# Optimization experiments

Hardware: AMD Instinct MI355X
Metric: run time of the kernel (lower is better)

The kernel has to match this reference:

```python
import jax, jax.numpy as jnp
import numpy as np

EPS = 1e-8  # torch.nn.CosineSimilarity default eps


def _one_sided_chamfer(ex, ey):
    # ex: [N, D], ey: [M, D]
    # cosine(ex_i, ey_j) = <ex_i, ey_j> / (max(||ex_i||, eps) * max(||ey_j||, eps))
    nx = jnp.maximum(jnp.linalg.norm(ex, axis=-1, keepdims=True), EPS)  # [N,1]
    ny = jnp.maximum(jnp.linalg.norm(ey, axis=-1, keepdims=True), EPS)  # [M,1]
    exn = ex / nx
    eyn = ey / ny
    sims = jnp.einsum('nd,md->nm', exn, eyn)  # [N, M] cosine matrix
    return jnp.max(sims, axis=-1)  # row-wise max -> [N]


def setup_inputs() -> dict:
    key = jax.random.key(0)
    k1, k2 = jax.random.split(key)
    ex = jax.random.normal(k1, (8192, 768), dtype=jnp.float32)
    ey = jax.random.normal(k2, (8192, 768), dtype=jnp.float32)
    return {"ex": ex, "ey": ey}


def reference(ex, ey):
    return _one_sided_chamfer(ex, ey)
```

## Files before the change

kernel.cpp:

```cpp
#include <hip/hip_runtime.h>
#include <math.h>

#define NROWS 8192
#define KDIM  768
#define BM 128
#define BN 128
#define BKB 128
#define KTILES (KDIM / BKB)
#define NBC 4
#define NBCG (NROWS / BN / NBC)

typedef int i32x4 __attribute__((ext_vector_type(4)));

static __device__ __forceinline__ unsigned enc_f(float f) {
    unsigned x = __float_as_uint(f);
    return (x & 0x80000000u) ? ~x : (x | 0x80000000u);
}
static __device__ __forceinline__ float dec_f(unsigned u) {
    unsigned x = (u & 0x80000000u) ? (u ^ 0x80000000u) : ~u;
    return __uint_as_float(x);
}

__global__ __launch_bounds__(256) void normalize_quant_k(
        const float* __restrict__ ex, const float* __restrict__ ey,
        signed char* __restrict__ q, float* __restrict__ scales,
        unsigned* __restrict__ out) {
    if (blockIdx.x < NROWS / 256)
        out[blockIdx.x * 256 + threadIdx.x] = enc_f(-INFINITY);
    const int wave = threadIdx.x >> 6, lane = threadIdx.x & 63;
    const int grow = blockIdx.x * 4 + wave;
    const float* src = (grow < NROWS) ? ex : ey;
    const int row = grow & (NROWS - 1);
    const float4* xr = (const float4*)(src + (size_t)row * KDIM);
    float4 v[3];
    #pragma unroll
    for (int g = 0; g < 3; ++g) v[g] = xr[lane + g * 64];
    float ss = 0.f, am = 0.f;
    #pragma unroll
    for (int g = 0; g < 3; ++g) {
        ss += v[g].x * v[g].x + v[g].y * v[g].y + v[g].z * v[g].z + v[g].w * v[g].w;
        am = fmaxf(am, fmaxf(fmaxf(fabsf(v[g].x), fabsf(v[g].y)),
                             fmaxf(fabsf(v[g].z), fabsf(v[g].w))));
    }
    #pragma unroll
    for (int off = 32; off > 0; off >>= 1) {
        ss += __shfl_xor(ss, off);
        am = fmaxf(am, __shfl_xor(am, off));
    }
    const float scale = 1.0f / fmaxf(sqrtf(ss), 1e-8f);
    am = fmaxf(am * scale, 1e-12f);
    if (lane == 0) scales[grow] = am * (1.0f / 127.0f);
    const float si = scale * (127.0f / am);
    int* dr = (int*)(q + (size_t)grow * KDIM);
    #pragma unroll
    for (int g = 0; g < 3; ++g) {
        int qx = min(127, max(-127, __float2int_rn(v[g].x * si)));
        int qy = min(127, max(-127, __float2int_rn(v[g].y * si)));
        int qz = min(127, max(-127, __float2int_rn(v[g].z * si)));
        int qw = min(127, max(-127, __float2int_rn(v[g].w * si)));
        dr[lane + g * 64] = (qx & 0xff) | ((qy & 0xff) << 8) |
                            ((qz & 0xff) << 16) | ((qw & 0xff) << 24);
    }
}

__global__ __launch_bounds__(256, 4) void gemm_rowmax_i8_k(
        const signed char* __restrict__ A, const signed char* __restrict__ B,
        const float* __restrict__ sa, const float* __restrict__ sb,
        unsigned* __restrict__ out) {
    __shared__ signed char As[BM * BKB];
    __shared__ signed char Bs[BN * BKB];

    const int tid  = threadIdx.x;
    const int wave = tid >> 6, lane = tid & 63;
    const int br  = blockIdx.x >> 4;
    const int bcg = blockIdx.x & 15;

    const int srow   = lane >> 3;
    const int gchunk = (lane & 7) ^ srow;
    const int scol   = gchunk * 16;
    const signed char* aStage = A + (size_t)(br * BM + wave * 8 + srow) * KDIM + scol;
    signed char* lA = As + wave * 1024;
    signed char* lB = Bs + wave * 1024;

    const int wm = (wave >> 1) * 64, wn = (wave & 1) * 64;
    const int quad = lane >> 4, mrow = lane & 15;
    const int c0 = quad ^ (mrow & 7);
    const signed char* aBase = As + (wm + mrow) * BKB;
    const signed char* bBase = Bs + (wn + mrow) * BKB;
    const int row0 = br * BM + wm + quad * 4;

    #pragma unroll 1
    for (int bi = 0; bi < NBC; ++bi) {
        const int bc = bcg * NBC + bi;
        const signed char* bStage =
            B + (size_t)(bc * BN + wave * 8 + srow) * KDIM + scol;

        i32x4 acc[4][4] = {};

        #pragma unroll 1
        for (int kt = 0; kt < KTILES; ++kt) {
            __syncthreads();
            #pragma unroll
            for (int i = 0; i < 4; ++i) {
                __builtin_amdgcn_global_load_lds(
                    (const __attribute__((address_space(1))) void*)(aStage + kt * BKB + i * 24576),
                    (__attribute__((address_space(3))) void*)(lA + i * 4096), 16, 0, 0);
                __builtin_amdgcn_global_load_lds(
                    (const __attribute__((address_space(1))) void*)(bStage + kt * BKB + i * 24576),
                    (__attribute__((address_space(3))) void*)(lB + i * 4096), 16, 0, 0);
            }
            __syncthreads();

            #pragma unroll 1
            for (int ks = 0; ks < 2; ++ks) {
                const int ck = c0 ^ (ks << 2);
                i32x4 af[4], bfr[4];
                #pragma unroll
                for (int mi = 0; mi < 4; ++mi)
                    af[mi] = *(const i32x4*)(aBase + mi * 16 * BKB + ck * 16);
                #pragma unroll
                for (int ni = 0; ni < 4; ++ni)
                    bfr[ni] = *(const i32x4*)(bBase + ni * 16 * BKB + ck * 16);
                #pragma unroll
                for (int mi = 0; mi < 4; ++mi)
                    #pragma unroll
                    for (int ni = 0; ni < 4; ++ni)
                        acc[mi][ni] = __builtin_amdgcn_mfma_i32_16x16x64_i8(
                            af[mi], bfr[ni], acc[mi][ni], 0, 0, 0);
            }
        }

        float sbv[4];
        #pragma unroll
        for (int ni = 0; ni < 4; ++ni)
            sbv[ni] = sb[bc * BN + wn + ni * 16 + mrow];
        #pragma unroll
        for (int mi = 0; mi < 4; ++mi) {
            #pragma unroll
            for (int r = 0; r < 4; ++r) {
                float v = fmaxf(fmaxf((float)acc[mi][0][r] * sbv[0],
                                      (float)acc[mi][1][r] * sbv[1]),
                                fmaxf((float)acc[mi][2][r] * sbv[2],
                                      (float)acc[mi][3][r] * sbv[3]));
                v = fmaxf(v, __shfl_xor(v, 1));
                v = fmaxf(v, __shfl_xor(v, 2));
                v = fmaxf(v, __shfl_xor(v, 4));
                v = fmaxf(v, __shfl_xor(v, 8));
                if (mrow == 0) {
                    const int row = row0 + mi * 16 + r;
                    atomicMax(&out[row], enc_f(v * sa[row]));
                }
            }
        }
    }
}

__global__ void decode_out_k(unsigned* __restrict__ u) {
    int i = blockIdx.x * 256 + threadIdx.x;
    ((float*)u)[i] = dec_f(u[i]);
}

extern "C" void kernel_launch(void* const* d_in, const int* in_sizes, int n_in,
                              void* d_out, int out_size, void* d_ws, size_t ws_size,
                              hipStream_t stream) {
    (void)in_sizes; (void)n_in; (void)out_size; (void)ws_size;
    const float* ex = (const float*)d_in[0];
    const float* ey = (const float*)d_in[1];
    signed char* q = (signed char*)d_ws;
    float* scales  = (float*)(q + 2 * (size_t)NROWS * KDIM);
    unsigned* outu = (unsigned*)d_out;

    normalize_quant_k<<<(2 * NROWS) / 4, 256, 0, stream>>>(ex, ey, q, scales, outu);
    gemm_rowmax_i8_k<<<(NROWS / BM) * NBCG, 256, 0, stream>>>(
        q, q + (size_t)NROWS * KDIM, scales, scales + NROWS, outu);
    decode_out_k<<<NROWS / 256, 256, 0, stream>>>(outu);
}
```

Measured before the change: 165.3 us.

## Enlarge int8 GEMM tiles to 256x256 with 4-stage async LDS pipeline

Doubles the block tile to 256x256 with 512 threads (8 waves, each computing 128x64) and halves the K step to 64. Global-to-LDS loads now run three stages ahead through a four-buffer ring, gated by explicit vmcnt waits and a single barrier per step instead of two syncthreads. The goal is to hide load latency and raise arithmetic intensity. In exchange, LDS use and register pressure grow, and the grid shrinks to 256 blocks, which may underfill the GPU.

```diff
diff --git a/kernel.cpp b/kernel.cpp
--- a/kernel.cpp
+++ b/kernel.cpp
@@ -3,12 +3,12 @@
 
 #define NROWS 8192
 #define KDIM  768
-#define BM 128
-#define BN 128
-#define BKB 128
-#define KTILES (KDIM / BKB)
+#define BM 256
+#define BN 256
+#define BKB 64
+#define KT (KDIM / BKB)
 #define NBC 4
-#define NBCG (NROWS / BN / NBC)
+#define NT_ALL (NBC * KT)
 
 typedef int i32x4 __attribute__((ext_vector_type(4)));
 
@@ -63,79 +63,89 @@
     }
 }
 
-__global__ __launch_bounds__(256, 4) void gemm_rowmax_i8_k(
+__global__ __launch_bounds__(512, 2) void gemm_rowmax_i8_k(
         const signed char* __restrict__ A, const signed char* __restrict__ B,
         const float* __restrict__ sa, const float* __restrict__ sb,
         unsigned* __restrict__ out) {
-    __shared__ signed char As[BM * BKB];
-    __shared__ signed char Bs[BN * BKB];
+    __shared__ __attribute__((aligned(128))) signed char As[4][BM * BKB];
+    __shared__ __attribute__((aligned(128))) signed char Bs[4][BN * BKB];
 
     const int tid  = threadIdx.x;
     const int wave = tid >> 6, lane = tid & 63;
-    const int br  = blockIdx.x >> 4;
-    const int bcg = blockIdx.x & 15;
+    const int br  = blockIdx.x >> 3;
+    const int bcg = blockIdx.x & 7;
 
-    const int srow   = lane >> 3;
-    const int gchunk = (lane & 7) ^ srow;
-    const int scol   = gchunk * 16;
-    const signed char* aStage = A + (size_t)(br * BM + wave * 8 + srow) * KDIM + scol;
-    signed char* lA = As + wave * 1024;
-    signed char* lB = Bs + wave * 1024;
+    const int srow   = lane >> 2;
+    const int gchunk = (lane & 3) ^ (srow & 3);
+    const size_t aRowBase =
+        (size_t)(br * BM + wave * 32 + srow) * KDIM + gchunk * 16;
+    const int ldsW = wave * 2048;
 
-    const int wm = (wave >> 1) * 64, wn = (wave & 1) * 64;
+    const int wm = (wave >> 2) * 128, wn = (wave & 3) * 64;
     const int quad = lane >> 4, mrow = lane & 15;
-    const int c0 = quad ^ (mrow & 7);
-    const signed char* aBase = As + (wm + mrow) * BKB;
-    const signed char* bBase = Bs + (wn + mrow) * BKB;
-    const int row0 = br * BM + wm + quad * 4;
+    const int rslot = quad ^ (mrow & 3);
+
+    #define STAGE(sidx) do {                                                          \
+        const int s_ = (sidx);                                                        \
+        const int bi_ = s_ / KT, kt_ = s_ % KT;                                       \
+        const signed char* ag = A + aRowBase + kt_ * BKB;                             \
+        const signed char* bg = B + (size_t)((bcg * NBC + bi_) * BN + wave * 32 + srow) * KDIM \
+                                  + gchunk * 16 + kt_ * BKB;                          \
+        signed char* la = &As[s_ & 3][ldsW];                                          \
+        signed char* lb = &Bs[s_ & 3][ldsW];                                          \
+        __builtin_amdgcn_global_load_lds((const __attribute__((address_space(1))) void*)ag, \
+            (__attribute__((address_space(3))) void*)la, 16, 0, 0);                   \
+        __builtin_amdgcn_global_load_lds((const __attribute__((address_space(1))) void*)(ag + 16 * KDIM), \
+            (__attribute__((address_space(3))) void*)(la + 1024), 16, 0, 0);          \
+        __builtin_amdgcn_global_load_lds((const __attribute__((address_space(1))) void*)bg, \
+            (__attribute__((address_space(3))) void*)lb, 16, 0, 0);                   \
+        __builtin_amdgcn_global_load_lds((const __attribute__((address_space(1))) void*)(bg + 16 * KDIM), \
+            (__attribute__((address_space(3))) void*)(lb + 1024), 16, 0, 0);          \
+    } while (0)
+
+    STAGE(0); STAGE(1); STAGE(2);
+    int s = 3, t = 0;
 
     #pragma unroll 1
     for (int bi = 0; bi < NBC; ++bi) {
-        const int bc = bcg * NBC + bi;
-        const signed char* bStage =
-            B + (size_t)(bc * BN + wave * 8 + srow) * KDIM + scol;
+        i32x4 acc[8][4] = {};
+        #pragma unroll 1
+        for (int kt = 0; kt < KT; ++kt, ++t) {
+            if (t < NT_ALL - 2)       asm volatile("s_waitcnt vmcnt(8)" ::: "memory");
+            else if (t == NT_ALL - 2) asm volatile("s_waitcnt vmcnt(4)" ::: "memory");
+            else                      asm volatile("s_waitcnt vmcnt(0)" ::: "memory");
+            __builtin_amdgcn_s_barrier();
+            __builtin_amdgcn_sched_barrier(0);
 
-        i32x4 acc[4][4] = {};
+            if (s < NT_ALL) { STAGE(s); ++s; }
 
-        #pragma unroll 1
-        for (int kt = 0; kt < KTILES; ++kt) {
-            __syncthreads();
+            const int cb = t & 3;
+            const signed char* aB = &As[cb][(wm + mrow) * BKB + rslot * 16];
+            const signed char* bB = &Bs[cb][(wn + mrow) * BKB + rslot * 16];
+            i32x4 af[8], bf[4];
             #pragma unroll
-            for (int i = 0; i < 4; ++i) {
-                __builtin_amdgcn_global_load_lds(
-                    (const __attribute__((address_space(1))) void*)(aStage + kt * BKB + i * 24576),
-                    (__attribute__((address_space(3))) void*)(lA + i * 4096), 16, 0, 0);
-                __builtin_amdgcn_global_load_lds(
-                    (const __attribute__((address_space(1))) void*)(bStage + kt * BKB + i * 24576),
-                    (__attribute__((address_space(3))) void*)(lB + i * 4096), 16, 0, 0);
-            }
-            __syncthreads();
+            for (int mi = 0; mi < 8; ++mi) af[mi] = *(const i32x4*)(aB + mi * 16 * BKB);
+            #pragma unroll
+            for (int ni = 0; ni < 4; ++ni) bf[ni] = *(const i32x4*)(bB + ni * 16 * BKB);
 
-            #pragma unroll 1
-            for (int ks = 0; ks < 2; ++ks) {
-                const int ck = c0 ^ (ks << 2);
-                i32x4 af[4], bfr[4];
-                #pragma unroll
-                for (int mi = 0; mi < 4; ++mi)
-                    af[mi] = *(const i32x4*)(aBase + mi * 16 * BKB + ck * 16);
+            __builtin_amdgcn_s_setprio(1);
+            #pragma unroll
+            for (int mi = 0; mi < 8; ++mi)
                 #pragma unroll
                 for (int ni = 0; ni < 4; ++ni)
-                    bfr[ni] = *(const i32x4*)(bBase + ni * 16 * BKB + ck * 16);
-                #pragma unroll
-                for (int mi = 0; mi < 4; ++mi)
-                    #pragma unroll
-                    for (int ni = 0; ni < 4; ++ni)
-                        acc[mi][ni] = __builtin_amdgcn_mfma_i32_16x16x64_i8(
-                            af[mi], bfr[ni], acc[mi][ni], 0, 0, 0);
-            }
+                    acc[mi][ni] = __builtin_amdgcn_mfma_i32_16x16x64_i8(
+                        af[mi], bf[ni], acc[mi][ni], 0, 0, 0);
+            __builtin_amdgcn_s_setprio(0);
         }
 
+        const int bc = bcg * NBC + bi;
         float sbv[4];
         #pragma unroll
         for (int ni = 0; ni < 4; ++ni)
             sbv[ni] = sb[bc * BN + wn + ni * 16 + mrow];
+        const int row0 = br * BM + wm + quad * 4;
         #pragma unroll
-        for (int mi = 0; mi < 4; ++mi) {
+        for (int mi = 0; mi < 8; ++mi) {
             #pragma unroll
             for (int r = 0; r < 4; ++r) {
                 float v = fmaxf(fmaxf((float)acc[mi][0][r] * sbv[0],
@@ -153,6 +163,7 @@
             }
         }
     }
+    #undef STAGE
 }
 
 __global__ void decode_out_k(unsigned* __restrict__ u) {
@@ -171,7 +182,7 @@
     unsigned* outu = (unsigned*)d_out;
 
     normalize_quant_k<<<(2 * NROWS) / 4, 256, 0, stream>>>(ex, ey, q, scales, outu);
-    gemm_rowmax_i8_k<<<(NROWS / BM) * NBCG, 256, 0, stream>>>(
+    gemm_rowmax_i8_k<<<(NROWS / BM) * (NROWS / BN / NBC), 512, 0, stream>>>(
         q, q + (size_t)NROWS * KDIM, scales, scales + NROWS, outu);
     decode_out_k<<<NROWS / 256, 256, 0, stream>>>(outu);
 }
```

Measured after the change: 202.4 us. 1.22x slower.
